# Optimization experiments

Measured on AMD Instinct MI355X. Metric: run time of the kernel, lower is better.

## Reference

```python
import jax, jax.numpy as jnp
import numpy as np

D = 1024
H = 16
HD = D // H
EPS = 1e-8


def setup_inputs() -> dict:
    key = jax.random.key(0)
    ks = jax.random.split(key, 12)
    B, S = 2, 2048
    scale = 1.0 / np.sqrt(D)
    inp = {
        "x": jax.random.normal(ks[0], (B, S, D), dtype=jnp.float32),
        "M": jax.random.uniform(ks[1], (B, S, S), dtype=jnp.float32),
        "Wq": jax.random.normal(ks[2], (D, D), dtype=jnp.float32) * scale,
        "bq": jax.random.normal(ks[3], (D,), dtype=jnp.float32) * 0.01,
        "Wk": jax.random.normal(ks[4], (D, D), dtype=jnp.float32) * scale,
        "bk": jax.random.normal(ks[5], (D,), dtype=jnp.float32) * 0.01,
        "Wv": jax.random.normal(ks[6], (D, D), dtype=jnp.float32) * scale,
        "bv": jax.random.normal(ks[7], (D,), dtype=jnp.float32) * 0.01,
        "Wo": jax.random.normal(ks[8], (D, D), dtype=jnp.float32) * scale,
        "bo": jax.random.normal(ks[9], (D,), dtype=jnp.float32) * 0.01,
    }
    return inp


def reference(x, M, Wq, bq, Wk, bk, Wv, bv, Wo, bo):
    B, S, _ = x.shape
    sm_scale = HD ** -0.5
    # projections (torch Linear: x @ W^T + b), split into heads: [B,H,S,HD]
    def proj(W, b):
        return (x @ W.T + b).reshape(B, S, H, HD).transpose(0, 2, 1, 3)
    Q, K, V = proj(Wq, bq), proj(Wk, bk), proj(Wv, bv)
    # scores: [B,H,S,S], gated pre-softmax by M broadcast over heads
    scores = jnp.einsum("bhqd,bhkd->bhqk", Q, K) * sm_scale
    Mb = M[:, None, :, :]  # [B,1,S,S]
    scores = scores * Mb
    attn = jax.nn.softmax(scores, axis=-1)
    # post-softmax re-gate + L1 renormalize
    A_sparse = attn * Mb
    norm = jnp.sum(jnp.abs(A_sparse), axis=-1, keepdims=True) + EPS
    A_bar = A_sparse / norm
    out = jnp.einsum("bhqk,bhkd->bhqd", A_bar, V)
    out = out.transpose(0, 2, 1, 3).reshape(B, S, D)
    return out @ Wo.T + bo
```

## Files before the change

### kernel.cpp

```cpp
#include <hip/hip_runtime.h>
#include <hip/hip_bf16.h>
#include <stdint.h>

#define S_LEN 2048
#define D_DIM 1024
#define NROW 4096

typedef __attribute__((ext_vector_type(8))) short short8;
typedef __attribute__((ext_vector_type(4))) float f32x4;
typedef __attribute__((ext_vector_type(4))) int i32x4;
typedef unsigned short ushort_t;

__device__ __forceinline__ ushort_t f2bf(float f) {
  uint32_t u = __float_as_uint(f);
  u += 0x7fffu + ((u >> 16) & 1u);
  return (ushort_t)(u >> 16);
}

__device__ __forceinline__ void gload16(const void* g, void* l) {
  __builtin_amdgcn_global_load_lds((const __attribute__((address_space(1))) void*)g,
                                   (__attribute__((address_space(3))) void*)l, 16, 0, 0);
}

__global__ void convert4_kernel(const float* __restrict__ x,
                                const float* __restrict__ wq, const float* __restrict__ wk,
                                const float* __restrict__ wv,
                                ushort_t* __restrict__ xb, ushort_t* __restrict__ wcat) {
  const float* src; ushort_t* dst; int n;
  switch (blockIdx.y) {
    case 0: src = x;  dst = xb;             n = NROW * D_DIM;  break;
    case 1: src = wq; dst = wcat;           n = D_DIM * D_DIM; break;
    case 2: src = wk; dst = wcat + 1048576; n = D_DIM * D_DIM; break;
    default: src = wv; dst = wcat + 2097152; n = D_DIM * D_DIM; break;
  }
  int base = (blockIdx.x * 256 + threadIdx.x) * 8;
  if (base >= n) return;
  f32x4 va = *(const f32x4*)(src + base);
  f32x4 vb = *(const f32x4*)(src + base + 4);
  short8 o;
  o[0] = (short)f2bf(va[0]); o[1] = (short)f2bf(va[1]);
  o[2] = (short)f2bf(va[2]); o[3] = (short)f2bf(va[3]);
  o[4] = (short)f2bf(vb[0]); o[5] = (short)f2bf(vb[1]);
  o[6] = (short)f2bf(vb[2]); o[7] = (short)f2bf(vb[3]);
  *(short8*)(dst + base) = o;
}

__global__ void convert_wo_kernel(const float* __restrict__ wo, ushort_t* __restrict__ wob) {
  int base = (blockIdx.x * 256 + threadIdx.x) * 8;
  f32x4 va = *(const f32x4*)(wo + base);
  f32x4 vb = *(const f32x4*)(wo + base + 4);
  short8 o;
  o[0] = (short)f2bf(va[0]); o[1] = (short)f2bf(va[1]);
  o[2] = (short)f2bf(va[2]); o[3] = (short)f2bf(va[3]);
  o[4] = (short)f2bf(vb[0]); o[5] = (short)f2bf(vb[1]);
  o[6] = (short)f2bf(vb[2]); o[7] = (short)f2bf(vb[3]);
  *(short8*)(wob + base) = o;
}

template<int MODE>
__global__ __launch_bounds__(256, 4) void gemm_glds(const ushort_t* __restrict__ A,
                                                    const ushort_t* __restrict__ Bw,
                                                    const float* __restrict__ bias0,
                                                    const float* __restrict__ bias1,
                                                    const float* __restrict__ bias2,
                                                    void* __restrict__ Cout) {
  __shared__ ushort_t As[128 * 64];
  __shared__ ushort_t Bs[128 * 64];
  const int t = threadIdx.x;
  const int lane = t & 63;
  const int w = t >> 6;
  const int wm = w >> 1, wn = w & 1;
  const int m0 = blockIdx.x * 128, n0 = blockIdx.y * 128;
  const int g = lane >> 4, c0 = lane & 15;
  const int srow = lane >> 3, scol = (lane & 7) * 8;

  f32x4 acc[4][4] = {};

  for (int kt = 0; kt < 16; ++kt) {
    const int kk = kt * 64;
#pragma unroll
    for (int i = 0; i < 4; ++i) {
      gload16(A  + (size_t)(m0 + w * 32 + i * 8 + srow) * D_DIM + kk + scol, &As[(w * 32 + i * 8) * 64]);
      gload16(Bw + (size_t)(n0 + w * 32 + i * 8 + srow) * D_DIM + kk + scol, &Bs[(w * 32 + i * 8) * 64]);
    }
    asm volatile("s_waitcnt vmcnt(0)" ::: "memory");
    __syncthreads();
#pragma unroll
    for (int kc = 0; kc < 2; ++kc) {
      short8 af[4], bf[4];
#pragma unroll
      for (int mf = 0; mf < 4; ++mf)
        af[mf] = *(const short8*)&As[(wm * 64 + mf * 16 + c0) * 64 + kc * 32 + g * 8];
#pragma unroll
      for (int nf = 0; nf < 4; ++nf)
        bf[nf] = *(const short8*)&Bs[(wn * 64 + nf * 16 + c0) * 64 + kc * 32 + g * 8];
#pragma unroll
      for (int mf = 0; mf < 4; ++mf)
#pragma unroll
        for (int nf = 0; nf < 4; ++nf)
          acc[mf][nf] = __builtin_amdgcn_mfma_f32_16x16x32_bf16(af[mf], bf[nf], acc[mf][nf], 0, 0, 0);
    }
    __syncthreads();
  }

#pragma unroll
  for (int nf = 0; nf < 4; ++nf) {
    int jj = n0 + wn * 64 + nf * 16 + c0;
    float bval;
    if (MODE == 0) {
      int proj = jj >> 10, jcol = jj & 1023;
      const float* bp = (proj == 0) ? bias0 : ((proj == 1) ? bias1 : bias2);
      bval = bp[jcol];
    } else {
      bval = bias0[jj];
    }
#pragma unroll
    for (int mf = 0; mf < 4; ++mf) {
#pragma unroll
      for (int r = 0; r < 4; ++r) {
        int ii = m0 + wm * 64 + mf * 16 + g * 4 + r;
        float v = acc[mf][nf][r] + bval;
        if (MODE == 2) {
          ((float*)Cout)[(size_t)ii * D_DIM + jj] = v;
        } else {
          int proj = jj >> 10, jcol = jj & 1023;
          if (proj == 0) v *= 0.125f;
          int bb = ii >> 11, s = ii & 2047;
          size_t addr;
          if (proj == 0) {
            int hcol = jcol >> 6, hd = jcol & 63;
            addr = ((size_t)(bb * 16 + hcol) * 2048 + s) * 64 + hd;
          } else if (proj == 1) {
            int hcol = jcol >> 6, hd = jcol & 63;
            addr = (size_t)4194304 + ((size_t)(bb * 16 + hcol) * 2048 + s) * 64
                 + (hd ^ ((s & 7) << 3));
          } else {
            addr = (size_t)8388608 + ((size_t)bb * 1024 + jcol) * 2048
                 + (s ^ ((jcol & 7) << 3));
          }
          ((ushort_t*)Cout)[addr] = f2bf(v);
        }
      }
    }
  }
}

__global__ __launch_bounds__(512, 4) void attn_kernel(const ushort_t* __restrict__ Qg,
                                                      const ushort_t* __restrict__ Kg,
                                                      const ushort_t* __restrict__ Vtg,
                                                      const float* __restrict__ Mg,
                                                      ushort_t* __restrict__ aout) {
  __shared__ ushort_t Ks[2][64 * 64];
  __shared__ ushort_t Vts[2][64 * 64];

  const int t = threadIdx.x, lane = t & 63, w = t >> 6;
  const int g = lane >> 4, c0 = lane & 15;
  const int id = blockIdx.x;
  const int r8 = id & 7, hh = (id >> 3) & 15, ss = id >> 7;
  const int combo = r8 + 8 * ss, b = combo >> 4, q0 = (combo & 15) * 128;
  const int bh = b * 16 + hh;

  const ushort_t* Qbase = Qg + ((size_t)bh * 2048 + q0) * 64;
  const float*    Mbase = Mg + ((size_t)b * 2048 + q0 + w * 16 + c0) * 2048 + g * 4;

  const ushort_t* Ksrc = Kg  + (size_t)bh * 2048 * 64
                       + ((size_t)(w * 8 + (lane >> 3)) * 64 + (lane & 7) * 8);
  const ushort_t* Vsrc = Vtg + (size_t)bh * 64 * 2048
                       + ((size_t)(w * 8 + (lane >> 3)) * 2048 + (lane & 7) * 8);

  short8 qf[2];
#pragma unroll
  for (int kc = 0; kc < 2; ++kc)
    qf[kc] = *(const short8*)(Qbase + (size_t)(w * 16 + c0) * 64 + kc * 32 + g * 8);

  f32x4 o[4] = {};
  f32x4 dpev = {0.f, 0.f, 0.f, 0.f};
  const int swz = (c0 & 7) << 3;
  const int idxA = (((g & 1) * 2 + (g >> 1)) * 16 + c0) * 4;
  const int idxB = (((g & 1) * 2 + 1 - (g >> 1)) * 16 + c0) * 4;
  const bool glo = (g < 2);
  const bool gb = (g & 1);

#define STAGE(kt_, buf_) { \
    gload16(Ksrc + (size_t)(kt_) * 4096, &Ks[buf_][w * 512]); \
    gload16(Vsrc + (size_t)(kt_) * 64,   &Vts[buf_][w * 512]); }

  STAGE(0, 0);
  f32x4 rm[4];
#pragma unroll
  for (int nf = 0; nf < 4; ++nf) rm[nf] = *(const f32x4*)(Mbase + nf * 16);
  asm volatile("s_waitcnt vmcnt(0)" ::: "memory");
  __builtin_amdgcn_s_barrier();
  __builtin_amdgcn_sched_barrier(0);

  for (int kt = 0; kt < 32; ++kt) {
    const int cur = kt & 1;
    f32x4 rmn[4];
    if (kt < 31) {
      STAGE(kt + 1, cur ^ 1);
      __builtin_amdgcn_sched_barrier(0);
      const float* Mk = Mbase + (size_t)(kt + 1) * 64;
#pragma unroll
      for (int nf = 0; nf < 4; ++nf) rmn[nf] = *(const f32x4*)(Mk + nf * 16);
    }

    f32x4 sf[4] = {};
    __builtin_amdgcn_s_setprio(1);
#pragma unroll
    for (int kc = 0; kc < 2; ++kc) {
      short8 kf[4];
#pragma unroll
      for (int nf = 0; nf < 4; ++nf)
        kf[nf] = *(const short8*)&Ks[cur][(nf * 16 + c0) * 64 + ((kc * 32 + g * 8) ^ swz)];
#pragma unroll
      for (int nf = 0; nf < 4; ++nf)
        sf[nf] = __builtin_amdgcn_mfma_f32_16x16x32_bf16(kf[nf], qf[kc], sf[nf], 0, 0, 0);
    }
    __builtin_amdgcn_s_setprio(0);

    uint32_t w4[4][2];
#pragma unroll
    for (int nf = 0; nf < 4; ++nf) {
      float p[4];
#pragma unroll
      for (int r = 0; r < 4; ++r) {
        float m = rm[nf][r];
        float e = __expf(sf[nf][r] * m);
        float pe = m * e;
        dpev[r] += pe;
        p[r] = pe;
      }
      asm("v_cvt_pk_bf16_f32 %0, %1, %2" : "=v"(w4[nf][0]) : "v"(p[0]), "v"(p[1]));
      asm("v_cvt_pk_bf16_f32 %0, %1, %2" : "=v"(w4[nf][1]) : "v"(p[2]), "v"(p[3]));
    }

    short8 pf[2];
#pragma unroll
    for (int kc = 0; kc < 2; ++kc) {
      uint32_t sA0 = gb ? w4[2 * kc + 1][0] : w4[2 * kc][0];
      uint32_t sA1 = gb ? w4[2 * kc + 1][1] : w4[2 * kc][1];
      uint32_t sB0 = gb ? w4[2 * kc][0]     : w4[2 * kc + 1][0];
      uint32_t sB1 = gb ? w4[2 * kc][1]     : w4[2 * kc + 1][1];
      uint32_t rA0 = (uint32_t)__builtin_amdgcn_ds_bpermute(idxA, (int)sA0);
      uint32_t rA1 = (uint32_t)__builtin_amdgcn_ds_bpermute(idxA, (int)sA1);
      uint32_t rB0 = (uint32_t)__builtin_amdgcn_ds_bpermute(idxB, (int)sB0);
      uint32_t rB1 = (uint32_t)__builtin_amdgcn_ds_bpermute(idxB, (int)sB1);
      i32x4 f4;
      f4[0] = (int)(glo ? rA0 : rB0);
      f4[1] = (int)(glo ? rA1 : rB1);
      f4[2] = (int)(glo ? rB0 : rA0);
      f4[3] = (int)(glo ? rB1 : rA1);
      pf[kc] = __builtin_bit_cast(short8, f4);
    }

    __builtin_amdgcn_s_setprio(1);
#pragma unroll
    for (int kc = 0; kc < 2; ++kc) {
#pragma unroll
      for (int df = 0; df < 4; ++df) {
        short8 vf = *(const short8*)&Vts[cur][(df * 16 + c0) * 64 + ((kc * 32 + g * 8) ^ swz)];
        o[df] = __builtin_amdgcn_mfma_f32_16x16x32_bf16(vf, pf[kc], o[df], 0, 0, 0);
      }
    }
    __builtin_amdgcn_s_setprio(0);

    if (kt < 31) {
      asm volatile("s_waitcnt vmcnt(4)" ::: "memory");
      __builtin_amdgcn_s_barrier();
      __builtin_amdgcn_sched_barrier(0);
#pragma unroll
      for (int nf = 0; nf < 4; ++nf) rm[nf] = rmn[nf];
    }
  }

  float dpe = (dpev[0] + dpev[1]) + (dpev[2] + dpev[3]);
  dpe += __shfl_xor(dpe, 16);
  dpe += __shfl_xor(dpe, 32);
  float inv = 1.0f / dpe;

#pragma unroll
  for (int df = 0; df < 4; ++df) {
    float v0 = o[df][0] * inv, v1 = o[df][1] * inv;
    float v2 = o[df][2] * inv, v3 = o[df][3] * inv;
    uint32_t d0, d1;
    asm("v_cvt_pk_bf16_f32 %0, %1, %2" : "=v"(d0) : "v"(v0), "v"(v1));
    asm("v_cvt_pk_bf16_f32 %0, %1, %2" : "=v"(d1) : "v"(v2), "v"(v3));
    unsigned long long pk = (unsigned long long)d0 | ((unsigned long long)d1 << 32);
    *(unsigned long long*)&aout[((size_t)b * 2048 + q0 + w * 16 + c0) * 1024 + hh * 64 + df * 16 + g * 4] = pk;
  }
#undef STAGE
}

extern "C" void kernel_launch(void* const* d_in, const int* in_sizes, int n_in,
                              void* d_out, int out_size, void* d_ws, size_t ws_size,
                              hipStream_t stream) {
  const float* x  = (const float*)d_in[0];
  const float* M  = (const float*)d_in[1];
  const float* Wq = (const float*)d_in[2];
  const float* bq = (const float*)d_in[3];
  const float* Wk = (const float*)d_in[4];
  const float* bk = (const float*)d_in[5];
  const float* Wv = (const float*)d_in[6];
  const float* bv = (const float*)d_in[7];
  const float* Wo = (const float*)d_in[8];
  const float* bo = (const float*)d_in[9];
  float* out = (float*)d_out;
  char* ws = (char*)d_ws;

  ushort_t* Qb    = (ushort_t*)(ws);
  ushort_t* Kb    = (ushort_t*)(ws + 8388608);
  ushort_t* Vtb   = (ushort_t*)(ws + 16777216);
  ushort_t* xb    = (ushort_t*)(ws + 25165824);
  ushort_t* Wcat  = (ushort_t*)(ws + 33554432);
  ushort_t* aoutb = (ushort_t*)(ws + 41943040);
  ushort_t* wob   = (ushort_t*)(ws + 39845888);

  convert4_kernel<<<dim3(2048, 4), 256, 0, stream>>>(x, Wq, Wk, Wv, xb, Wcat);
  convert_wo_kernel<<<512, 256, 0, stream>>>(Wo, wob);
  gemm_glds<0><<<dim3(32, 24), 256, 0, stream>>>(xb, Wcat, bq, bk, bv, (void*)Qb);
  attn_kernel<<<512, 512, 0, stream>>>(Qb, Kb, Vtb, M, aoutb);
  gemm_glds<2><<<dim3(32, 8), 256, 0, stream>>>(aoutb, wob, bo, bo, bo, (void*)out);
}
```

Baseline: 151.1 us.

## Pre-pack mask into fp16 fragment-ordered layout and use exp2 with folded scale

Measured after the change: 161.8 us. 7.1% more time.

```diff
diff --git a/kernel.cpp b/kernel.cpp
--- a/kernel.cpp
+++ b/kernel.cpp
@@ -9,12 +9,18 @@
 typedef __attribute__((ext_vector_type(8))) short short8;
 typedef __attribute__((ext_vector_type(4))) float f32x4;
 typedef __attribute__((ext_vector_type(4))) int i32x4;
+typedef __attribute__((ext_vector_type(8))) _Float16 h8;
 typedef unsigned short ushort_t;
 
 __device__ __forceinline__ ushort_t f2bf(float f) {
   uint32_t u = __float_as_uint(f);
   u += 0x7fffu + ((u >> 16) & 1u);
   return (ushort_t)(u >> 16);
+}
+
+__device__ __forceinline__ ushort_t f2h(float f) {
+  _Float16 h = (_Float16)f;
+  return __builtin_bit_cast(ushort_t, h);
 }
 
 __device__ __forceinline__ void gload16(const void* g, void* l) {
@@ -55,6 +61,25 @@
   o[4] = (short)f2bf(vb[0]); o[5] = (short)f2bf(vb[1]);
   o[6] = (short)f2bf(vb[2]); o[7] = (short)f2bf(vb[3]);
   *(short8*)(wob + base) = o;
+}
+
+__global__ __launch_bounds__(256) void m2_transform(const float* __restrict__ M,
+                                                    ushort_t* __restrict__ M2) {
+  int tid = blockIdx.x * 256 + threadIdx.x;
+  int lane = tid & 63, w = (tid >> 6) & 7, kt = (tid >> 9) & 31, combo = tid >> 14;
+  int c0 = lane & 15, g = lane >> 4;
+  int b = combo >> 4, q0i = combo & 15;
+  const float* src = M + ((size_t)b * 2048 + q0i * 128 + w * 16 + c0) * 2048 + kt * 64 + g * 4;
+  ushort_t outv[16];
+#pragma unroll
+  for (int nf = 0; nf < 4; ++nf) {
+    f32x4 v = *(const f32x4*)(src + nf * 16);
+#pragma unroll
+    for (int r = 0; r < 4; ++r)
+      outv[nf * 4 + r] = f2h(v[r]);
+  }
+  *(short8*)(M2 + (size_t)tid * 16)     = *(short8*)&outv[0];
+  *(short8*)(M2 + (size_t)tid * 16 + 8) = *(short8*)&outv[8];
 }
 
 template<int MODE>
@@ -124,7 +149,7 @@
           ((float*)Cout)[(size_t)ii * D_DIM + jj] = v;
         } else {
           int proj = jj >> 10, jcol = jj & 1023;
-          if (proj == 0) v *= 0.125f;
+          if (proj == 0) v *= 0.18033688011112042f;
           int bb = ii >> 11, s = ii & 2047;
           size_t addr;
           if (proj == 0) {
@@ -148,7 +173,7 @@
 __global__ __launch_bounds__(512, 4) void attn_kernel(const ushort_t* __restrict__ Qg,
                                                       const ushort_t* __restrict__ Kg,
                                                       const ushort_t* __restrict__ Vtg,
-                                                      const float* __restrict__ Mg,
+                                                      const ushort_t* __restrict__ M2,
                                                       ushort_t* __restrict__ aout) {
   __shared__ ushort_t Ks[2][64 * 64];
   __shared__ ushort_t Vts[2][64 * 64];
@@ -160,18 +185,18 @@
   const int combo = r8 + 8 * ss, b = combo >> 4, q0 = (combo & 15) * 128;
   const int bh = b * 16 + hh;
 
-  const ushort_t* Qbase = Qg + ((size_t)bh * 2048 + q0) * 64;
-  const float*    Mbase = Mg + ((size_t)b * 2048 + q0 + w * 16 + c0) * 2048 + g * 4;
+  const ushort_t* Qbase  = Qg + ((size_t)bh * 2048 + q0) * 64;
+  const ushort_t* M2base = M2 + ((size_t)combo * 32 * 8 + w) * 64 * 16 + (size_t)lane * 16;
+
+  short8 qf[2];
+#pragma unroll
+  for (int kc = 0; kc < 2; ++kc)
+    qf[kc] = *(const short8*)(Qbase + (size_t)(w * 16 + c0) * 64 + kc * 32 + g * 8);
 
   const ushort_t* Ksrc = Kg  + (size_t)bh * 2048 * 64
                        + ((size_t)(w * 8 + (lane >> 3)) * 64 + (lane & 7) * 8);
   const ushort_t* Vsrc = Vtg + (size_t)bh * 64 * 2048
                        + ((size_t)(w * 8 + (lane >> 3)) * 2048 + (lane & 7) * 8);
-
-  short8 qf[2];
-#pragma unroll
-  for (int kc = 0; kc < 2; ++kc)
-    qf[kc] = *(const short8*)(Qbase + (size_t)(w * 16 + c0) * 64 + kc * 32 + g * 8);
 
   f32x4 o[4] = {};
   f32x4 dpev = {0.f, 0.f, 0.f, 0.f};
@@ -186,22 +211,20 @@
     gload16(Vsrc + (size_t)(kt_) * 64,   &Vts[buf_][w * 512]); }
 
   STAGE(0, 0);
-  f32x4 rm[4];
-#pragma unroll
-  for (int nf = 0; nf < 4; ++nf) rm[nf] = *(const f32x4*)(Mbase + nf * 16);
+  short8 rm0 = *(const short8*)(M2base);
+  short8 rm1 = *(const short8*)(M2base + 8);
   asm volatile("s_waitcnt vmcnt(0)" ::: "memory");
   __builtin_amdgcn_s_barrier();
   __builtin_amdgcn_sched_barrier(0);
 
   for (int kt = 0; kt < 32; ++kt) {
     const int cur = kt & 1;
-    f32x4 rmn[4];
+    short8 rm0n, rm1n;
     if (kt < 31) {
       STAGE(kt + 1, cur ^ 1);
       __builtin_amdgcn_sched_barrier(0);
-      const float* Mk = Mbase + (size_t)(kt + 1) * 64;
-#pragma unroll
-      for (int nf = 0; nf < 4; ++nf) rmn[nf] = *(const f32x4*)(Mk + nf * 16);
+      rm0n = *(const short8*)(M2base + (size_t)(kt + 1) * 8192);
+      rm1n = *(const short8*)(M2base + (size_t)(kt + 1) * 8192 + 8);
     }
 
     f32x4 sf[4] = {};
@@ -218,14 +241,16 @@
     }
     __builtin_amdgcn_s_setprio(0);
 
+    h8 mh0 = __builtin_bit_cast(h8, rm0);
+    h8 mh1 = __builtin_bit_cast(h8, rm1);
     uint32_t w4[4][2];
 #pragma unroll
     for (int nf = 0; nf < 4; ++nf) {
       float p[4];
 #pragma unroll
       for (int r = 0; r < 4; ++r) {
-        float m = rm[nf][r];
-        float e = __expf(sf[nf][r] * m);
+        float m = (nf < 2) ? (float)mh0[nf * 4 + r] : (float)mh1[(nf - 2) * 4 + r];
+        float e = exp2f(sf[nf][r] * m);
         float pe = m * e;
         dpev[r] += pe;
         p[r] = pe;
@@ -265,11 +290,10 @@
     __builtin_amdgcn_s_setprio(0);
 
     if (kt < 31) {
-      asm volatile("s_waitcnt vmcnt(4)" ::: "memory");
+      asm volatile("s_waitcnt vmcnt(2)" ::: "memory");
       __builtin_amdgcn_s_barrier();
       __builtin_amdgcn_sched_barrier(0);
-#pragma unroll
-      for (int nf = 0; nf < 4; ++nf) rm[nf] = rmn[nf];
+      rm0 = rm0n; rm1 = rm1n;
     }
   }
 
@@ -312,12 +336,14 @@
   ushort_t* Vtb   = (ushort_t*)(ws + 16777216);
   ushort_t* xb    = (ushort_t*)(ws + 25165824);
   ushort_t* Wcat  = (ushort_t*)(ws + 33554432);
+  ushort_t* M2    = (ushort_t*)(ws + 25165824);
   ushort_t* aoutb = (ushort_t*)(ws + 41943040);
-  ushort_t* wob   = (ushort_t*)(ws + 39845888);
+  ushort_t* wob   = (ushort_t*)(ws);
 
   convert4_kernel<<<dim3(2048, 4), 256, 0, stream>>>(x, Wq, Wk, Wv, xb, Wcat);
+  gemm_glds<0><<<dim3(32, 24), 256, 0, stream>>>(xb, Wcat, bq, bk, bv, (void*)Qb);
+  m2_transform<<<2048, 256, 0, stream>>>(M, M2);
+  attn_kernel<<<512, 512, 0, stream>>>(Qb, Kb, Vtb, M2, aoutb);
   convert_wo_kernel<<<512, 256, 0, stream>>>(Wo, wob);
-  gemm_glds<0><<<dim3(32, 24), 256, 0, stream>>>(xb, Wcat, bq, bk, bv, (void*)Qb);
-  attn_kernel<<<512, 512, 0, stream>>>(Qb, Kb, Vtb, M, aoutb);
   gemm_glds<2><<<dim3(32, 8), 256, 0, stream>>>(aoutb, wob, bo, bo, bo, (void*)out);
 }
```
